# Kernel tuning notes

Hardware: AMD Instinct MI355X
Metric: run time of the kernel (lower is better)

Reference implementation:

```python
import jax, jax.numpy as jnp
import numpy as np

KERNEL_SIZE = (8,)

def setup_inputs() -> dict:
    key = jax.random.key(0)
    k1, = jax.random.split(key, 1)
    inputs = jax.random.normal(k1, (32, 131072, 8), dtype=jnp.float32)
    w = jnp.ones(KERNEL_SIZE, dtype=jnp.float32)  # initializer='ones', non-trainable
    return {"inputs": inputs, "w": w}

def reference(inputs, w):
    # keys[b, n] = sum_c inputs[b, n, c] * w[c]
    keys = jnp.einsum('bnc,c->bn', inputs, w)
    idx = jnp.argsort(keys, axis=-1)                     # [B, N] int
    # batched gather: out[b, i, :] = inputs[b, idx[b, i], :]
    out = jnp.take_along_axis(inputs, idx[:, :, None], axis=1)
    return out
```

## Files before the change

kernel.cpp:

```cpp
#include <hip/hip_runtime.h>


#define NB   32
#define NPB  131072
#define NK   (NB * NPB)
#define TPB  256
#define EPT  16
#define EPB  (TPB * EPT)
#define BPB  (NPB / EPB)
#define NBLK (NB * BPB)
#define BINS 256

typedef unsigned long long u64;
typedef unsigned int u32;

__device__ __forceinline__ u32 fkey(float x) {
    u32 u = __float_as_uint(x);
    return u ^ ((u & 0x80000000u) ? 0xFFFFFFFFu : 0x80000000u);
}

__device__ __forceinline__ u64 matchany(u32 d) {
    u64 m = ~0ull;
    #pragma unroll
    for (int k = 0; k < 8; ++k) {
        u64 bk = __ballot((d >> k) & 1u);
        m &= ((d >> k) & 1u) ? bk : ~bk;
    }
    return m;
}

__global__ void khist0(const float* __restrict__ in, const float* __restrict__ w,
                       u64* __restrict__ outp, u32* __restrict__ hist)
{
    __shared__ u32 h[BINS];
    int t = threadIdx.x;
    h[t] = 0;
    __syncthreads();
    int b = blockIdx.x / BPB, blk = blockIdx.x % BPB;
    size_t base = (size_t)b * NPB + (size_t)blk * EPB;
    int lane = t & 63;
    float w0 = w[0], w1 = w[1], w2 = w[2], w3 = w[3];
    float w4 = w[4], w5 = w[5], w6 = w[6], w7 = w[7];
    #pragma unroll
    for (int i = 0; i < EPT; ++i) {
        size_t row = base + t + i * TPB;
        const float4* p = (const float4*)in + row * 2;
        float4 a = p[0], c = p[1];
        float k = __fmul_rn(a.x, w0);
        k = __fadd_rn(k, __fmul_rn(a.y, w1));
        k = __fadd_rn(k, __fmul_rn(a.z, w2));
        k = __fadd_rn(k, __fmul_rn(a.w, w3));
        k = __fadd_rn(k, __fmul_rn(c.x, w4));
        k = __fadd_rn(k, __fmul_rn(c.y, w5));
        k = __fadd_rn(k, __fmul_rn(c.z, w6));
        k = __fadd_rn(k, __fmul_rn(c.w, w7));
        u32 fk = fkey(k);
        outp[row] = ((u64)fk << 32) | (u64)((u32)row & (NPB - 1));
        u32 d = fk & 255u;
        u64 m = matchany(d);
        if (lane == __ffsll(m) - 1) atomicAdd(&h[d], (u32)__popcll(m));
    }
    __syncthreads();
    hist[(b * BINS + t) * BPB + blk] = h[t];
}

__global__ void rhist(const u64* __restrict__ src, u32* __restrict__ hist, int shift)
{
    __shared__ u32 h[BINS];
    int t = threadIdx.x;
    h[t] = 0;
    __syncthreads();
    int b = blockIdx.x / BPB, blk = blockIdx.x % BPB;
    size_t base = (size_t)b * NPB + (size_t)blk * EPB;
    int lane = t & 63;
    #pragma unroll
    for (int i = 0; i < EPT; ++i) {
        u64 v = src[base + t + i * TPB];
        u32 d = (u32)(v >> shift) & 255u;
        u64 m = matchany(d);
        if (lane == __ffsll(m) - 1) atomicAdd(&h[d], (u32)__popcll(m));
    }
    __syncthreads();
    hist[(b * BINS + t) * BPB + blk] = h[t];
}

__global__ void rhist32(const u32* __restrict__ src, u32* __restrict__ hist)
{
    __shared__ u32 h[BINS];
    int t = threadIdx.x;
    h[t] = 0;
    __syncthreads();
    int b = blockIdx.x / BPB, blk = blockIdx.x % BPB;
    size_t base = (size_t)b * NPB + (size_t)blk * EPB;
    int lane = t & 63;
    #pragma unroll
    for (int i = 0; i < EPT; ++i) {
        u32 v = src[base + t + i * TPB];
        u32 d = v >> 24;
        u64 m = matchany(d);
        if (lane == __ffsll(m) - 1) atomicAdd(&h[d], (u32)__popcll(m));
    }
    __syncthreads();
    hist[(b * BINS + t) * BPB + blk] = h[t];
}

__global__ void rscan(u32* __restrict__ hist)
{
    int b = blockIdx.x, t = threadIdx.x;
    u32* H = hist + b * BINS * BPB;
    u32 v[32], s = 0;
    #pragma unroll
    for (int k = 0; k < 32; ++k) { v[k] = H[t * 32 + k]; s += v[k]; }
    int lane = t & 63, wid = t >> 6;
    u32 inc = s;
    #pragma unroll
    for (int off = 1; off < 64; off <<= 1) {
        u32 y = __shfl_up(inc, off, 64);
        if (lane >= off) inc += y;
    }
    __shared__ u32 wsum[4];
    if (lane == 63) wsum[wid] = inc;
    __syncthreads();
    u32 wo = 0;
    #pragma unroll
    for (int wI = 0; wI < 4; ++wI) if (wI < wid) wo += wsum[wI];
    u32 run = wo + inc - s;
    #pragma unroll
    for (int k = 0; k < 32; ++k) { u32 c = v[k]; H[t * 32 + k] = run; run += c; }
}

#define RANK_PERMUTE_BODY(SRC_EXPR)                                             \
    int t = threadIdx.x, lane = t & 63, wid = t >> 6;                           \
    size_t base = (size_t)b * NPB + (size_t)blk * EPB + (size_t)wid * 1024;     \
    _Pragma("unroll")                                                           \
    for (int k = 0; k < 4; ++k) ((u32*)s_wcnt)[t + k * TPB] = 0;                \
    __syncthreads();                                                            \
    u64 v[EPT];                                                                 \
    u32 rnk[EPT];                                                               \
    _Pragma("unroll")                                                           \
    for (int i = 0; i < EPT; ++i) v[i] = (SRC_EXPR);                            \
    _Pragma("unroll")                                                           \
    for (int i = 0; i < EPT; ++i) {                                             \
        u32 d = (u32)(v[i] >> shift) & 255u;                                    \
        u64 m = matchany(d);                                                    \
        int leader = __ffsll(m) - 1;                                            \
        u32 baseCnt = 0;                                                        \
        if (lane == leader) {                                                   \
            baseCnt = s_wcnt[wid][d];                                           \
            s_wcnt[wid][d] = baseCnt + (u32)__popcll(m);                        \
        }                                                                       \
        baseCnt = __shfl(baseCnt, leader, 64);                                  \
        rnk[i] = baseCnt + (u32)__popcll(m & ((1ull << lane) - 1ull));          \
        __builtin_amdgcn_wave_barrier();                                        \
    }                                                                           \
    __syncthreads();                                                            \
    u32 c0 = s_wcnt[0][t], c1 = s_wcnt[1][t], c2 = s_wcnt[2][t], c3 = s_wcnt[3][t]; \
    u32 tot = c0 + c1 + c2 + c3;                                                \
    s_wcnt[0][t] = 0; s_wcnt[1][t] = c0; s_wcnt[2][t] = c0 + c1;                \
    s_wcnt[3][t] = c0 + c1 + c2;                                                \
    u32 inc = tot;                                                              \
    _Pragma("unroll")                                                           \
    for (int off = 1; off < 64; off <<= 1) {                                    \
        u32 y = __shfl_up(inc, off, 64);                                        \
        if (lane >= off) inc += y;                                              \
    }                                                                           \
    if (lane == 63) s_wsum[wid] = inc;                                          \
    __syncthreads();                                                            \
    u32 wo = 0;                                                                 \
    _Pragma("unroll")                                                           \
    for (int wI = 0; wI < 4; ++wI) if (wI < wid) wo += s_wsum[wI];              \
    s_dbase[t] = wo + inc - tot;                                                \
    s_gbase[t] = hist[(b * BINS + t) * BPB + blk];                              \
    __syncthreads();                                                            \
    _Pragma("unroll")                                                           \
    for (int i = 0; i < EPT; ++i) {                                             \
        u32 d = (u32)(v[i] >> shift) & 255u;                                    \
        u32 pos = s_dbase[d] + s_wcnt[wid][d] + rnk[i];                         \
        s_key[pos] = (u32)(v[i] >> 32);                                         \
        s_idx[pos] = (u32)v[i];                                                 \
    }                                                                           \
    __syncthreads();

__launch_bounds__(TPB, 4)
__global__ void rscatter(const u64* __restrict__ src, u64* __restrict__ dst,
                         const u32* __restrict__ hist, int shift)
{
    __shared__ u32 s_key[EPB];
    __shared__ u32 s_idx[EPB];
    __shared__ u32 s_wcnt[4][BINS];
    __shared__ u32 s_dbase[BINS];
    __shared__ u32 s_gbase[BINS];
    __shared__ u32 s_wsum[4];
    int b = blockIdx.x / BPB, blk = blockIdx.x % BPB;
    RANK_PERMUTE_BODY(src[base + i * 64 + lane])

    int kshift = shift - 32;
    #pragma unroll
    for (int i = 0; i < EPT; ++i) {
        int j = i * TPB + t;
        u32 key = s_key[j], idx = s_idx[j];
        u32 d = (key >> kshift) & 255u;
        u32 gpos = s_gbase[d] + (u32)j - s_dbase[d];
        dst[(size_t)b * NPB + gpos] = ((u64)key << 32) | (u64)idx;
    }
}

__launch_bounds__(TPB, 4)
__global__ void rscat2c(const u64* __restrict__ src, u32* __restrict__ dstc,
                        const u32* __restrict__ hist)
{
    __shared__ u32 s_key[EPB];
    __shared__ u32 s_idx[EPB];
    __shared__ u32 s_wcnt[4][BINS];
    __shared__ u32 s_dbase[BINS];
    __shared__ u32 s_gbase[BINS];
    __shared__ u32 s_wsum[4];
    const int shift = 48;
    int b = blockIdx.x / BPB, blk = blockIdx.x % BPB;
    RANK_PERMUTE_BODY(src[base + i * 64 + lane])

    #pragma unroll
    for (int i = 0; i < EPT; ++i) {
        int j = i * TPB + t;
        u32 key = s_key[j], idx = s_idx[j];
        u32 d = (key >> 16) & 255u;
        u32 gpos = s_gbase[d] + (u32)j - s_dbase[d];
        dstc[(size_t)b * NPB + gpos] = (key & 0xFF000000u) | idx;
    }
}

__launch_bounds__(TPB, 6)
__global__ void rscatgat32(const u32* __restrict__ src, const float* __restrict__ in,
                           float* __restrict__ out, const u32* __restrict__ hist)
{
    __shared__ u32 s_pack[EPB];
    __shared__ u32 s_wcnt[4][BINS];
    __shared__ u32 s_dbase[BINS];
    __shared__ u32 s_gbase[BINS];
    __shared__ u32 s_wsum[4];
    int i0 = blockIdx.x;
    int xcd = i0 & 7, j0 = i0 >> 3;
    int b = xcd + 8 * (j0 >> 5), blk = j0 & 31;

    int t = threadIdx.x, lane = t & 63, wid = t >> 6;
    size_t base = (size_t)b * NPB + (size_t)blk * EPB + (size_t)wid * 1024;
    #pragma unroll
    for (int k = 0; k < 4; ++k) ((u32*)s_wcnt)[t + k * TPB] = 0;
    __syncthreads();

    u32 v[EPT];
    u32 rnk[EPT];
    #pragma unroll
    for (int i = 0; i < EPT; ++i) v[i] = src[base + i * 64 + lane];

    #pragma unroll
    for (int i = 0; i < EPT; ++i) {
        u32 d = v[i] >> 24;
        u64 m = matchany(d);
        int leader = __ffsll(m) - 1;
        u32 baseCnt = 0;
        if (lane == leader) {
            baseCnt = s_wcnt[wid][d];
            s_wcnt[wid][d] = baseCnt + (u32)__popcll(m);
        }
        baseCnt = __shfl(baseCnt, leader, 64);
        rnk[i] = baseCnt + (u32)__popcll(m & ((1ull << lane) - 1ull));
        __builtin_amdgcn_wave_barrier();
    }
    __syncthreads();

    u32 c0 = s_wcnt[0][t], c1 = s_wcnt[1][t], c2 = s_wcnt[2][t], c3 = s_wcnt[3][t];
    u32 tot = c0 + c1 + c2 + c3;
    s_wcnt[0][t] = 0; s_wcnt[1][t] = c0; s_wcnt[2][t] = c0 + c1; s_wcnt[3][t] = c0 + c1 + c2;
    u32 inc = tot;
    #pragma unroll
    for (int off = 1; off < 64; off <<= 1) {
        u32 y = __shfl_up(inc, off, 64);
        if (lane >= off) inc += y;
    }
    if (lane == 63) s_wsum[wid] = inc;
    __syncthreads();
    u32 wo = 0;
    #pragma unroll
    for (int wI = 0; wI < 4; ++wI) if (wI < wid) wo += s_wsum[wI];
    s_dbase[t] = wo + inc - tot;
    s_gbase[t] = hist[(b * BINS + t) * BPB + blk];
    __syncthreads();

    #pragma unroll
    for (int i = 0; i < EPT; ++i) {
        u32 d = v[i] >> 24;
        u32 pos = s_dbase[d] + s_wcnt[wid][d] + rnk[i];
        s_pack[pos] = v[i];
    }
    __syncthreads();

    const float4* inb = (const float4*)in + ((size_t)b << 18);
    float4* outb = (float4*)out + ((size_t)b << 18);
    #pragma unroll
    for (int i = 0; i < EPT; ++i) {
        int j = i * TPB + t;
        u32 pack = s_pack[j];
        u32 d = pack >> 24;
        u32 idx = pack & 0x1FFFFu;
        u32 gpos = s_gbase[d] + (u32)j - s_dbase[d];
        const float4* s = inb + (size_t)idx * 2;
        float4 x = s[0], y = s[1];
        float4* drow = outb + (size_t)gpos * 2;
        drow[0] = x; drow[1] = y;
    }
}

extern "C" void kernel_launch(void* const* d_in, const int* in_sizes, int n_in,
                              void* d_out, int out_size, void* d_ws, size_t ws_size,
                              hipStream_t stream)
{
    const float* in = (const float*)d_in[0];
    const float* w  = (const float*)d_in[1];
    float* out = (float*)d_out;

    u64* A   = (u64*)d_ws;
    u32* A32 = (u32*)d_ws;
    u64* B   = (u64*)d_out;
    u32* hist = (u32*)((char*)d_ws + (size_t)NK * 8);

    khist0<<<NBLK, TPB, 0, stream>>>(in, w, B, hist);
    rscan<<<NB, TPB, 0, stream>>>(hist);
    rscatter<<<NBLK, TPB, 0, stream>>>(B, A, hist, 32);

    rhist<<<NBLK, TPB, 0, stream>>>(A, hist, 40);
    rscan<<<NB, TPB, 0, stream>>>(hist);
    rscatter<<<NBLK, TPB, 0, stream>>>(A, B, hist, 40);

    rhist<<<NBLK, TPB, 0, stream>>>(B, hist, 48);
    rscan<<<NB, TPB, 0, stream>>>(hist);
    rscat2c<<<NBLK, TPB, 0, stream>>>(B, A32, hist);

    rhist32<<<NBLK, TPB, 0, stream>>>(A32, hist);
    rscan<<<NB, TPB, 0, stream>>>(hist);
    rscatgat32<<<NBLK, TPB, 0, stream>>>(A32, in, out, hist);
}
```

Measured before the change: 234.1 us.

## Write 32-bit keys in first pass and replace final gather with rank scatter plus permute

The first pass now writes only 32-bit keys, and the row index is built inside the first scatter instead of being stored as 64-bit pairs. The final pass no longer stages data through shared memory and gathers input rows by index. It writes each element's destination rank to a buffer, and a separate permute kernel reads input rows in order and scatters them to their sorted positions. This turns random 32-byte reads into coalesced reads with random writes and cuts first-pass write traffic. The cost is an extra kernel launch, an extra rank buffer round trip, and random 4-byte rank writes.

```diff
diff --git a/kernel.cpp b/kernel.cpp
--- a/kernel.cpp
+++ b/kernel.cpp
@@ -30,7 +30,7 @@
 }
 
 __global__ void khist0(const float* __restrict__ in, const float* __restrict__ w,
-                       u64* __restrict__ outp, u32* __restrict__ hist)
+                       u32* __restrict__ keyout, u32* __restrict__ hist)
 {
     __shared__ u32 h[BINS];
     int t = threadIdx.x;
@@ -55,7 +55,7 @@
         k = __fadd_rn(k, __fmul_rn(c.z, w6));
         k = __fadd_rn(k, __fmul_rn(c.w, w7));
         u32 fk = fkey(k);
-        outp[row] = ((u64)fk << 32) | (u64)((u32)row & (NPB - 1));
+        keyout[row] = fk;
         u32 d = fk & 255u;
         u64 m = matchany(d);
         if (lane == __ffsll(m) - 1) atomicAdd(&h[d], (u32)__popcll(m));
@@ -182,6 +182,31 @@
     __syncthreads();
 
 __launch_bounds__(TPB, 4)
+__global__ void rscat0(const u32* __restrict__ keys, u64* __restrict__ dst,
+                       const u32* __restrict__ hist)
+{
+    __shared__ u32 s_key[EPB];
+    __shared__ u32 s_idx[EPB];
+    __shared__ u32 s_wcnt[4][BINS];
+    __shared__ u32 s_dbase[BINS];
+    __shared__ u32 s_gbase[BINS];
+    __shared__ u32 s_wsum[4];
+    const int shift = 32;
+    int b = blockIdx.x / BPB, blk = blockIdx.x % BPB;
+    RANK_PERMUTE_BODY(((u64)keys[base + i * 64 + lane] << 32) |
+                      (u64)((u32)(base + i * 64 + lane) & (NPB - 1)))
+
+    #pragma unroll
+    for (int i = 0; i < EPT; ++i) {
+        int j = i * TPB + t;
+        u32 key = s_key[j], idx = s_idx[j];
+        u32 d = key & 255u;
+        u32 gpos = s_gbase[d] + (u32)j - s_dbase[d];
+        dst[(size_t)b * NPB + gpos] = ((u64)key << 32) | (u64)idx;
+    }
+}
+
+__launch_bounds__(TPB, 4)
 __global__ void rscatter(const u64* __restrict__ src, u64* __restrict__ dst,
                          const u32* __restrict__ hist, int shift)
 {
@@ -229,21 +254,15 @@
     }
 }
 
-__launch_bounds__(TPB, 6)
-__global__ void rscatgat32(const u32* __restrict__ src, const float* __restrict__ in,
-                           float* __restrict__ out, const u32* __restrict__ hist)
-{
-    __shared__ u32 s_pack[EPB];
+__global__ void rscatrank(const u32* __restrict__ src, u32* __restrict__ rank,
+                          const u32* __restrict__ hist)
+{
     __shared__ u32 s_wcnt[4][BINS];
-    __shared__ u32 s_dbase[BINS];
     __shared__ u32 s_gbase[BINS];
-    __shared__ u32 s_wsum[4];
-    int i0 = blockIdx.x;
-    int xcd = i0 & 7, j0 = i0 >> 3;
-    int b = xcd + 8 * (j0 >> 5), blk = j0 & 31;
-
     int t = threadIdx.x, lane = t & 63, wid = t >> 6;
+    int b = blockIdx.x / BPB, blk = blockIdx.x % BPB;
     size_t base = (size_t)b * NPB + (size_t)blk * EPB + (size_t)wid * 1024;
+
     #pragma unroll
     for (int k = 0; k < 4; ++k) ((u32*)s_wcnt)[t + k * TPB] = 0;
     __syncthreads();
@@ -269,45 +288,38 @@
     }
     __syncthreads();
 
-    u32 c0 = s_wcnt[0][t], c1 = s_wcnt[1][t], c2 = s_wcnt[2][t], c3 = s_wcnt[3][t];
-    u32 tot = c0 + c1 + c2 + c3;
+    u32 c0 = s_wcnt[0][t], c1 = s_wcnt[1][t], c2 = s_wcnt[2][t];
     s_wcnt[0][t] = 0; s_wcnt[1][t] = c0; s_wcnt[2][t] = c0 + c1; s_wcnt[3][t] = c0 + c1 + c2;
-    u32 inc = tot;
-    #pragma unroll
-    for (int off = 1; off < 64; off <<= 1) {
-        u32 y = __shfl_up(inc, off, 64);
-        if (lane >= off) inc += y;
-    }
-    if (lane == 63) s_wsum[wid] = inc;
-    __syncthreads();
-    u32 wo = 0;
-    #pragma unroll
-    for (int wI = 0; wI < 4; ++wI) if (wI < wid) wo += s_wsum[wI];
-    s_dbase[t] = wo + inc - tot;
     s_gbase[t] = hist[(b * BINS + t) * BPB + blk];
     __syncthreads();
 
+    u32* rb = rank + (size_t)b * NPB;
     #pragma unroll
     for (int i = 0; i < EPT; ++i) {
         u32 d = v[i] >> 24;
-        u32 pos = s_dbase[d] + s_wcnt[wid][d] + rnk[i];
-        s_pack[pos] = v[i];
-    }
-    __syncthreads();
-
-    const float4* inb = (const float4*)in + ((size_t)b << 18);
+        u32 gpos = s_gbase[d] + s_wcnt[wid][d] + rnk[i];
+        rb[v[i] & 0x1FFFFu] = gpos;
+    }
+}
+
+__global__ void permute(const float* __restrict__ in, const u32* __restrict__ rank,
+                        float* __restrict__ out)
+{
+    int i0 = blockIdx.x;
+    int xcd = i0 & 7, j0 = i0 >> 3;
+    int b = xcd + 8 * (j0 >> 5), blk = j0 & 31;
+    int t = threadIdx.x;
+    size_t base = (size_t)b * NPB + (size_t)blk * EPB;
+    const float4* inb = (const float4*)in;
     float4* outb = (float4*)out + ((size_t)b << 18);
     #pragma unroll
     for (int i = 0; i < EPT; ++i) {
-        int j = i * TPB + t;
-        u32 pack = s_pack[j];
-        u32 d = pack >> 24;
-        u32 idx = pack & 0x1FFFFu;
-        u32 gpos = s_gbase[d] + (u32)j - s_dbase[d];
-        const float4* s = inb + (size_t)idx * 2;
+        size_t r = base + t + i * TPB;
+        u32 g = rank[r];
+        const float4* s = inb + r * 2;
         float4 x = s[0], y = s[1];
-        float4* drow = outb + (size_t)gpos * 2;
-        drow[0] = x; drow[1] = y;
+        float4* d = outb + (size_t)g * 2;
+        d[0] = x; d[1] = y;
     }
 }
 
@@ -319,24 +331,28 @@
     const float* w  = (const float*)d_in[1];
     float* out = (float*)d_out;
 
-    u64* A   = (u64*)d_ws;
-    u32* A32 = (u32*)d_ws;
-    u64* B   = (u64*)d_out;
+    u32* K32  = (u32*)d_ws;
+    u64* A64  = (u64*)d_out;
+    u64* B64  = (u64*)d_ws;
+    u32* C32  = (u32*)d_out;
+    u32* rank = (u32*)d_ws;
     u32* hist = (u32*)((char*)d_ws + (size_t)NK * 8);
 
-    khist0<<<NBLK, TPB, 0, stream>>>(in, w, B, hist);
+    khist0<<<NBLK, TPB, 0, stream>>>(in, w, K32, hist);
     rscan<<<NB, TPB, 0, stream>>>(hist);
-    rscatter<<<NBLK, TPB, 0, stream>>>(B, A, hist, 32);
-
-    rhist<<<NBLK, TPB, 0, stream>>>(A, hist, 40);
+    rscat0<<<NBLK, TPB, 0, stream>>>(K32, A64, hist);
+
+    rhist<<<NBLK, TPB, 0, stream>>>(A64, hist, 40);
     rscan<<<NB, TPB, 0, stream>>>(hist);
-    rscatter<<<NBLK, TPB, 0, stream>>>(A, B, hist, 40);
-
-    rhist<<<NBLK, TPB, 0, stream>>>(B, hist, 48);
+    rscatter<<<NBLK, TPB, 0, stream>>>(A64, B64, hist, 40);
+
+    rhist<<<NBLK, TPB, 0, stream>>>(B64, hist, 48);
     rscan<<<NB, TPB, 0, stream>>>(hist);
-    rscat2c<<<NBLK, TPB, 0, stream>>>(B, A32, hist);
-
-    rhist32<<<NBLK, TPB, 0, stream>>>(A32, hist);
+    rscat2c<<<NBLK, TPB, 0, stream>>>(B64, C32, hist);
+
+    rhist32<<<NBLK, TPB, 0, stream>>>(C32, hist);
     rscan<<<NB, TPB, 0, stream>>>(hist);
-    rscatgat32<<<NBLK, TPB, 0, stream>>>(A32, in, out, hist);
-}
+    rscatrank<<<NBLK, TPB, 0, stream>>>(C32, rank, hist);
+
+    permute<<<NBLK, TPB, 0, stream>>>(in, rank, out);
+}
```

After: 299.0 us. 27.7% more time.
